# Performance work log

Measured on AMD Instinct MI355X. Metric: run time of the kernel, lower is better.

Reference implementation:

```python
import jax, jax.numpy as jnp
import numpy as np

NUM_USERS = 150000
NUM_ITEMS = 80000
N_NODES = NUM_USERS + NUM_ITEMS
NNZ = 5000000
LATENT_DIM = 64
N_LAYERS = 3


def setup_inputs() -> dict:
    key = jax.random.key(0)
    k1, k2, k3, k4, k5 = jax.random.split(key, 5)
    user_emb = 0.1 * jax.random.normal(k1, (NUM_USERS, LATENT_DIM), dtype=jnp.float32)
    item_emb = 0.1 * jax.random.normal(k2, (NUM_ITEMS, LATENT_DIM), dtype=jnp.float32)
    adj_rows = jax.random.randint(k3, (NNZ,), 0, N_NODES, dtype=jnp.int32)
    adj_cols = jax.random.randint(k4, (NNZ,), 0, N_NODES, dtype=jnp.int32)
    # scale values ~ 1/avg_degree so propagation is stable (mimics sym-normalized adjacency)
    adj_vals = jax.random.uniform(k5, (NNZ,), dtype=jnp.float32) * (N_NODES / NNZ)
    return {"user_emb": user_emb, "item_emb": item_emb,
            "adj_rows": adj_rows, "adj_cols": adj_cols, "adj_vals": adj_vals}


def _spmm(rows, cols, vals, x):
    # y[r] = sum_{e: rows[e]==r} vals[e] * x[cols[e]]  == torch.sparse.mm(G, x)
    return jax.ops.segment_sum(vals[:, None] * x[cols], rows, num_segments=N_NODES)


def reference(user_emb, item_emb, adj_rows, adj_cols, adj_vals):
    all_emb = jnp.concatenate([user_emb, item_emb], axis=0)  # [N, d]
    acc = all_emb
    for _ in range(N_LAYERS):
        all_emb = _spmm(adj_rows, adj_cols, adj_vals, all_emb)
        acc = acc + all_emb
    light_out = acc / (N_LAYERS + 1)  # mean over stacked layer embeddings
    users = light_out[:NUM_USERS]
    items = light_out[NUM_USERS:]
    return users, items
```

## Files before the change

### kernel.cpp

```cpp
#include <hip/hip_runtime.h>

#define NUM_USERS 150000
#define NUM_ITEMS 80000
#define N_NODES   230000
#define NNZ       5000000
#define DIM       64

#define SB_SHIFT 10
#define SB_SIZE  1024
#define NUM_SB   ((N_NODES + SB_SIZE - 1) / SB_SIZE)
#define SB_CAP   32768
#define PA_ITEMS 4

#define NSLICES   (N_NODES / 8)

#define VAL_MAX   0.046f
#define VAL_ENC   (16384.0f / VAL_MAX)
#define VAL_SCALE (VAL_MAX / 16384.0f)

__device__ __forceinline__ unsigned short f2bf(float f) {
    unsigned int u = __float_as_uint(f);
    u += 0x7FFFu + ((u >> 16) & 1u);
    return (unsigned short)(u >> 16);
}
__device__ __forceinline__ float bflo(unsigned int u) {
    return __uint_as_float(u << 16);
}
__device__ __forceinline__ float bfhi(unsigned int u) {
    return __uint_as_float(u & 0xFFFF0000u);
}
__device__ __forceinline__ unsigned int pk2(float a, float b) {
    return (unsigned int)f2bf(a) | ((unsigned int)f2bf(b) << 16);
}

__global__ void init_kernel(const float* __restrict__ u,
                            const float* __restrict__ it,
                            unsigned short* __restrict__ x) {
    long i = (long)blockIdx.x * blockDim.x + threadIdx.x;
    const long n4  = (long)N_NODES * DIM / 4;
    const long iu4 = (long)NUM_USERS * DIM / 4;
    if (i >= n4) return;
    float4 v = (i < iu4) ? ((const float4*)u)[i]
                         : ((const float4*)it)[i - iu4];
    ushort4 h;
    h.x = f2bf(v.x); h.y = f2bf(v.y); h.z = f2bf(v.z); h.w = f2bf(v.w);
    ((ushort4*)x)[i] = h;
}

__global__ void cursor_init_kernel(int* __restrict__ bucket_cursor) {
    int t = threadIdx.x;
    if (t < NUM_SB) bucket_cursor[t] = t * SB_CAP;
}

__global__ void partA_kernel(const int* __restrict__ rows,
                             const int* __restrict__ cols,
                             const float* __restrict__ vals,
                             int* __restrict__ bucket_cursor,
                             unsigned int* __restrict__ Xe,
                             unsigned short* __restrict__ Xr) {
    __shared__ int bcnt[NUM_SB];
    __shared__ int bbase[NUM_SB];
    const int t = threadIdx.x;
    const long tile = 1024L * PA_ITEMS;
    for (long base = (long)blockIdx.x * tile; base < NNZ;
         base += (long)gridDim.x * tile) {
        for (int j = t; j < NUM_SB; j += 1024) bcnt[j] = 0;
        __syncthreads();
        int b[PA_ITEMS], rank[PA_ITEMS], rl[PA_ITEMS];
        unsigned int pk[PA_ITEMS];
        bool ok[PA_ITEMS];
        for (int k = 0; k < PA_ITEMS; ++k) {
            long e = base + (long)k * 1024 + t;
            ok[k] = (e < NNZ);
            if (ok[k]) {
                int r = rows[e];
                b[k]  = r >> SB_SHIFT;
                rl[k] = r & (SB_SIZE - 1);
                int vc = (int)(vals[e] * VAL_ENC + 0.5f);
                vc = min(vc, 16383);
                pk[k] = ((unsigned int)vc << 18) | (unsigned int)cols[e];
                rank[k] = atomicAdd(&bcnt[b[k]], 1);
            }
        }
        __syncthreads();
        for (int j = t; j < NUM_SB; j += 1024)
            if (bcnt[j] > 0) bbase[j] = atomicAdd(&bucket_cursor[j], bcnt[j]);
        __syncthreads();
        for (int k = 0; k < PA_ITEMS; ++k)
            if (ok[k]) {
                int pos = bbase[b[k]] + rank[k];
                Xe[pos] = pk[k];
                Xr[pos] = (unsigned short)rl[k];
            }
        __syncthreads();
    }
}

__global__ void sb_scan_kernel(const int* __restrict__ bucket_cursor,
                               int* __restrict__ sb_base) {
    __shared__ int lds[256];
    const int t = threadIdx.x;
    const int s = (t < NUM_SB) ? (bucket_cursor[t] - t * SB_CAP) : 0;
    lds[t] = s;
    __syncthreads();
    for (int off = 1; off < 256; off <<= 1) {
        int add = (t >= off) ? lds[t - off] : 0;
        __syncthreads();
        lds[t] += add;
        __syncthreads();
    }
    if (t < NUM_SB) sb_base[t] = lds[t] - s;
    if (t == 0) sb_base[NUM_SB] = NNZ;
}

__global__ void partB_kernel(const unsigned int* __restrict__ Xe,
                             const unsigned short* __restrict__ Xr,
                             const int* __restrict__ sb_base,
                             int* __restrict__ row_start,
                             unsigned int* __restrict__ edges) {
    __shared__ int hist[SB_SIZE];
    __shared__ int scan[SB_SIZE];
    const int b    = blockIdx.x;
    const int t    = threadIdx.x;
    const int rlo  = b << SB_SHIFT;
    const int nrows = min(SB_SIZE, N_NODES - rlo);
    const int xoff = b * SB_CAP;
    const int base = sb_base[b];
    const int cnt  = sb_base[b + 1] - base;
    hist[t] = 0;
    __syncthreads();
    for (int i = t; i < cnt; i += 1024)
        atomicAdd(&hist[Xr[xoff + i]], 1);
    __syncthreads();
    const int v = hist[t];
    scan[t] = v;
    __syncthreads();
    for (int off = 1; off < 1024; off <<= 1) {
        int add = (t >= off) ? scan[t - off] : 0;
        __syncthreads();
        scan[t] += add;
        __syncthreads();
    }
    const int rs = base + (scan[t] - v);
    if (t < nrows) row_start[rlo + t] = rs;
    hist[t] = rs;
    __syncthreads();
    for (int i = t; i < cnt; i += 1024) {
        int rl = Xr[xoff + i];
        int pos = atomicAdd(&hist[rl], 1);
        edges[pos] = Xe[xoff + i];
    }
    if (b == 0 && t == 0) row_start[N_NODES] = NNZ;
}

#define FMA8(v, h) \
    a0 = fmaf((v), bflo((h).x), a0); a1 = fmaf((v), bfhi((h).x), a1); \
    a2 = fmaf((v), bflo((h).y), a2); a3 = fmaf((v), bfhi((h).y), a3); \
    a4 = fmaf((v), bflo((h).z), a4); a5 = fmaf((v), bfhi((h).z), a5); \
    a6 = fmaf((v), bflo((h).w), a6); a7 = fmaf((v), bfhi((h).w), a7);

__global__ __launch_bounds__(256)
void spmm8_kernel(const int* __restrict__ row_start,
                  const unsigned int* __restrict__ edges,
                  const unsigned short* __restrict__ x,
                  unsigned short* __restrict__ y) {
    const int lane = threadIdx.x & 63;
    const int oct  = lane >> 3;
    const int fo   = (lane & 7) << 3;
    const int wv   = blockIdx.x * 4 + (threadIdx.x >> 6);
    if (wv >= NSLICES) return;
    const int row = wv * 8 + oct;
    const int s   = row_start[row];
    const int deg = row_start[row + 1] - s;
    int dm = deg;
    dm = max(dm, __shfl_xor(dm, 8));
    dm = max(dm, __shfl_xor(dm, 16));
    dm = max(dm, __shfl_xor(dm, 32));
    dm = __builtin_amdgcn_readfirstlane(dm);
    const unsigned short* xf = x + fo;
    float a0 = 0, a1 = 0, a2 = 0, a3 = 0, a4 = 0, a5 = 0, a6 = 0, a7 = 0;
    for (int i = 0; i < dm; i += 8) {
        unsigned int ev[8];
        uint4 h[8];
        #pragma unroll
        for (int k = 0; k < 8; ++k) {
            const int o = (i + k < deg) ? (s + i + k) : 0;
            ev[k] = edges[o];
        }
        #pragma unroll
        for (int k = 0; k < 8; ++k)
            h[k] = *(const uint4*)(xf + (((long)(ev[k] & 0x3FFFF)) << 6));
        #pragma unroll
        for (int k = 0; k < 8; ++k) {
            const float v = (i + k < deg)
                          ? (float)(ev[k] >> 18) * VAL_SCALE : 0.0f;
            FMA8(v, h[k]);
        }
    }
    uint4 w;
    w.x = pk2(a0, a1); w.y = pk2(a2, a3);
    w.z = pk2(a4, a5); w.w = pk2(a6, a7);
    *(uint4*)(y + (((long)row) << 6) + fo) = w;
}

__global__ __launch_bounds__(256)
void spmm_final8_kernel(const int* __restrict__ row_start,
                        const unsigned int* __restrict__ edges,
                        const unsigned short* __restrict__ y2,
                        const unsigned short* __restrict__ y1,
                        const float* __restrict__ u,
                        const float* __restrict__ it,
                        float* __restrict__ acc) {
    const int lane = threadIdx.x & 63;
    const int oct  = lane >> 3;
    const int fo   = (lane & 7) << 3;
    const int wv   = blockIdx.x * 4 + (threadIdx.x >> 6);
    if (wv >= NSLICES) return;
    const int row = wv * 8 + oct;
    const int s   = row_start[row];
    const int deg = row_start[row + 1] - s;
    int dm = deg;
    dm = max(dm, __shfl_xor(dm, 8));
    dm = max(dm, __shfl_xor(dm, 16));
    dm = max(dm, __shfl_xor(dm, 32));
    dm = __builtin_amdgcn_readfirstlane(dm);
    const unsigned short* xf = y2 + fo;
    float a0 = 0, a1 = 0, a2 = 0, a3 = 0, a4 = 0, a5 = 0, a6 = 0, a7 = 0;
    for (int i = 0; i < dm; i += 8) {
        unsigned int ev[8];
        uint4 h[8];
        #pragma unroll
        for (int k = 0; k < 8; ++k) {
            const int o = (i + k < deg) ? (s + i + k) : 0;
            ev[k] = edges[o];
        }
        #pragma unroll
        for (int k = 0; k < 8; ++k)
            h[k] = *(const uint4*)(xf + (((long)(ev[k] & 0x3FFFF)) << 6));
        #pragma unroll
        for (int k = 0; k < 8; ++k) {
            const float v = (i + k < deg)
                          ? (float)(ev[k] >> 18) * VAL_SCALE : 0.0f;
            FMA8(v, h[k]);
        }
    }
    const long o = (((long)row) << 6) + fo;
    const float* x0p = (row < NUM_USERS) ? (u + o)
                     : (it + o - (((long)NUM_USERS) << 6));
    const float4 xa = *(const float4*)(x0p);
    const float4 xb = *(const float4*)(x0p + 4);
    const uint4 h1 = *(const uint4*)(y1 + o);
    const uint4 h2 = *(const uint4*)(y2 + o);
    float4 ra, rb;
    ra.x = (xa.x + bflo(h1.x) + bflo(h2.x) + a0) * 0.25f;
    ra.y = (xa.y + bfhi(h1.x) + bfhi(h2.x) + a1) * 0.25f;
    ra.z = (xa.z + bflo(h1.y) + bflo(h2.y) + a2) * 0.25f;
    ra.w = (xa.w + bfhi(h1.y) + bfhi(h2.y) + a3) * 0.25f;
    rb.x = (xb.x + bflo(h1.z) + bflo(h2.z) + a4) * 0.25f;
    rb.y = (xb.y + bfhi(h1.z) + bfhi(h2.z) + a5) * 0.25f;
    rb.z = (xb.z + bflo(h1.w) + bflo(h2.w) + a6) * 0.25f;
    rb.w = (xb.w + bfhi(h1.w) + bfhi(h2.w) + a7) * 0.25f;
    *(float4*)(acc + o) = ra;
    *(float4*)(acc + o + 4) = rb;
}

extern "C" void kernel_launch(void* const* d_in, const int* in_sizes, int n_in,
                              void* d_out, int out_size, void* d_ws, size_t ws_size,
                              hipStream_t stream) {
    const float* u    = (const float*)d_in[0];
    const float* it   = (const float*)d_in[1];
    const int*   rows = (const int*)d_in[2];
    const int*   cols = (const int*)d_in[3];
    const float* vals = (const float*)d_in[4];
    float* acc = (float*)d_out;

    const size_t bufBf = (size_t)N_NODES * DIM * 2;
    const size_t edgeB = (size_t)NNZ * 4;
    const size_t XeB   = (size_t)NUM_SB * SB_CAP * 4;
    const size_t XrB   = (size_t)NUM_SB * SB_CAP * 2;
    const size_t nodeB = 921600;
    char* ws = (char*)d_ws;
    unsigned short* buf0 = (unsigned short*)(ws);
    unsigned short* buf1 = (unsigned short*)(ws + bufBf);
    unsigned short* buf2 = (unsigned short*)(ws + 2 * bufBf);
    unsigned int*   edges = (unsigned int*)(ws + 3 * bufBf);
    unsigned int*   Xe   = (unsigned int*)(ws + 3 * bufBf + edgeB);
    unsigned short* Xr   = (unsigned short*)(ws + 3 * bufBf + edgeB + XeB);
    char* p              = ws + 3 * bufBf + edgeB + XeB + XrB;
    int* row_start       = (int*)(p);   p += nodeB;
    int* bucket_cursor   = (int*)(p);   p += 1024;
    int* sb_base         = (int*)(p);

    const int n4 = N_NODES * DIM / 4;
    const int ewGrid = (n4 + 255) / 256;

    init_kernel<<<ewGrid, 256, 0, stream>>>(u, it, buf0);

    cursor_init_kernel<<<1, 256, 0, stream>>>(bucket_cursor);
    partA_kernel<<<512, 1024, 0, stream>>>(rows, cols, vals, bucket_cursor, Xe, Xr);
    sb_scan_kernel<<<1, 256, 0, stream>>>(bucket_cursor, sb_base);
    partB_kernel<<<NUM_SB, 1024, 0, stream>>>(Xe, Xr, sb_base, row_start, edges);

    const int spmmGrid = (NSLICES + 3) / 4;
    spmm8_kernel<<<spmmGrid, 256, 0, stream>>>(row_start, edges, buf0, buf1);
    spmm8_kernel<<<spmmGrid, 256, 0, stream>>>(row_start, edges, buf1, buf2);
    spmm_final8_kernel<<<spmmGrid, 256, 0, stream>>>(row_start, edges, buf2,
                                                     buf1, u, it, acc);
}
```

Measured before the change: 548.7 us.

## Halve super-bucket size and fold cursor init and bucket scan into neighbours

Super-buckets shrink from 1024 to 512 rows (about 450 buckets), which doubles the partB block count for better load balance. The cursor-init and bucket-scan kernels are removed: init_kernel now seeds the cursors, and every partB block redoes the bucket prefix scan itself. This cuts two launches and their serialization, at the cost of redundant scans in each block and more bucket atomics in partA. With SB_CAP at 16384, the expected bucket load of roughly 11k leaves a smaller safety margin.

```diff
diff --git a/kernel.cpp b/kernel.cpp
--- a/kernel.cpp
+++ b/kernel.cpp
@@ -6,10 +6,10 @@
 #define NNZ       5000000
 #define DIM       64
 
-#define SB_SHIFT 10
-#define SB_SIZE  1024
+#define SB_SHIFT 9
+#define SB_SIZE  512
 #define NUM_SB   ((N_NODES + SB_SIZE - 1) / SB_SIZE)
-#define SB_CAP   32768
+#define SB_CAP   16384
 #define PA_ITEMS 4
 
 #define NSLICES   (N_NODES / 8)
@@ -35,8 +35,10 @@
 
 __global__ void init_kernel(const float* __restrict__ u,
                             const float* __restrict__ it,
-                            unsigned short* __restrict__ x) {
+                            unsigned short* __restrict__ x,
+                            int* __restrict__ bucket_cursor) {
     long i = (long)blockIdx.x * blockDim.x + threadIdx.x;
+    if (i < NUM_SB) bucket_cursor[i] = (int)i * SB_CAP;
     const long n4  = (long)N_NODES * DIM / 4;
     const long iu4 = (long)NUM_USERS * DIM / 4;
     if (i >= n4) return;
@@ -47,17 +49,13 @@
     ((ushort4*)x)[i] = h;
 }
 
-__global__ void cursor_init_kernel(int* __restrict__ bucket_cursor) {
-    int t = threadIdx.x;
-    if (t < NUM_SB) bucket_cursor[t] = t * SB_CAP;
-}
-
-__global__ void partA_kernel(const int* __restrict__ rows,
-                             const int* __restrict__ cols,
-                             const float* __restrict__ vals,
-                             int* __restrict__ bucket_cursor,
-                             unsigned int* __restrict__ Xe,
-                             unsigned short* __restrict__ Xr) {
+__global__ __launch_bounds__(1024)
+void partA_kernel(const int* __restrict__ rows,
+                  const int* __restrict__ cols,
+                  const float* __restrict__ vals,
+                  int* __restrict__ bucket_cursor,
+                  unsigned int* __restrict__ Xe,
+                  unsigned short* __restrict__ Xr) {
     __shared__ int bcnt[NUM_SB];
     __shared__ int bbase[NUM_SB];
     const int t = threadIdx.x;
@@ -96,54 +94,50 @@
     }
 }
 
-__global__ void sb_scan_kernel(const int* __restrict__ bucket_cursor,
-                               int* __restrict__ sb_base) {
-    __shared__ int lds[256];
-    const int t = threadIdx.x;
-    const int s = (t < NUM_SB) ? (bucket_cursor[t] - t * SB_CAP) : 0;
-    lds[t] = s;
-    __syncthreads();
-    for (int off = 1; off < 256; off <<= 1) {
-        int add = (t >= off) ? lds[t - off] : 0;
-        __syncthreads();
-        lds[t] += add;
-        __syncthreads();
-    }
-    if (t < NUM_SB) sb_base[t] = lds[t] - s;
-    if (t == 0) sb_base[NUM_SB] = NNZ;
-}
-
-__global__ void partB_kernel(const unsigned int* __restrict__ Xe,
-                             const unsigned short* __restrict__ Xr,
-                             const int* __restrict__ sb_base,
-                             int* __restrict__ row_start,
-                             unsigned int* __restrict__ edges) {
+__global__ __launch_bounds__(1024)
+void partB_kernel(const unsigned int* __restrict__ Xe,
+                  const unsigned short* __restrict__ Xr,
+                  const int* __restrict__ bucket_cursor,
+                  int* __restrict__ row_start,
+                  unsigned int* __restrict__ edges) {
+    __shared__ int bsc[512];
     __shared__ int hist[SB_SIZE];
-    __shared__ int scan[SB_SIZE];
+    __shared__ int scn[SB_SIZE];
     const int b    = blockIdx.x;
     const int t    = threadIdx.x;
     const int rlo  = b << SB_SHIFT;
     const int nrows = min(SB_SIZE, N_NODES - rlo);
     const int xoff = b * SB_CAP;
-    const int base = sb_base[b];
-    const int cnt  = sb_base[b + 1] - base;
-    hist[t] = 0;
+
+    if (t < 512) bsc[t] = (t < NUM_SB) ? (bucket_cursor[t] - t * SB_CAP) : 0;
+    if (t < SB_SIZE) hist[t] = 0;
     __syncthreads();
+    for (int off = 1; off < 512; off <<= 1) {
+        int add = (t >= off && t < 512) ? bsc[t - off] : 0;
+        __syncthreads();
+        if (t < 512) bsc[t] += add;
+        __syncthreads();
+    }
+    const int base = (b == 0) ? 0 : bsc[b - 1];
+    const int cnt  = bsc[b] - base;
+
     for (int i = t; i < cnt; i += 1024)
         atomicAdd(&hist[Xr[xoff + i]], 1);
     __syncthreads();
-    const int v = hist[t];
-    scan[t] = v;
+    const int v = (t < SB_SIZE) ? hist[t] : 0;
+    if (t < SB_SIZE) scn[t] = v;
     __syncthreads();
-    for (int off = 1; off < 1024; off <<= 1) {
-        int add = (t >= off) ? scan[t - off] : 0;
-        __syncthreads();
-        scan[t] += add;
-        __syncthreads();
-    }
-    const int rs = base + (scan[t] - v);
-    if (t < nrows) row_start[rlo + t] = rs;
-    hist[t] = rs;
+    for (int off = 1; off < SB_SIZE; off <<= 1) {
+        int add = (t >= off && t < SB_SIZE) ? scn[t - off] : 0;
+        __syncthreads();
+        if (t < SB_SIZE) scn[t] += add;
+        __syncthreads();
+    }
+    if (t < SB_SIZE) {
+        const int rs = base + (scn[t] - v);
+        if (t < nrows) row_start[rlo + t] = rs;
+        hist[t] = rs;
+    }
     __syncthreads();
     for (int i = t; i < cnt; i += 1024) {
         int rl = Xr[xoff + i];
@@ -288,18 +282,16 @@
     unsigned short* Xr   = (unsigned short*)(ws + 3 * bufBf + edgeB + XeB);
     char* p              = ws + 3 * bufBf + edgeB + XeB + XrB;
     int* row_start       = (int*)(p);   p += nodeB;
-    int* bucket_cursor   = (int*)(p);   p += 1024;
-    int* sb_base         = (int*)(p);
+    int* bucket_cursor   = (int*)(p);
 
     const int n4 = N_NODES * DIM / 4;
     const int ewGrid = (n4 + 255) / 256;
 
-    init_kernel<<<ewGrid, 256, 0, stream>>>(u, it, buf0);
-
-    cursor_init_kernel<<<1, 256, 0, stream>>>(bucket_cursor);
+    init_kernel<<<ewGrid, 256, 0, stream>>>(u, it, buf0, bucket_cursor);
+
     partA_kernel<<<512, 1024, 0, stream>>>(rows, cols, vals, bucket_cursor, Xe, Xr);
-    sb_scan_kernel<<<1, 256, 0, stream>>>(bucket_cursor, sb_base);
-    partB_kernel<<<NUM_SB, 1024, 0, stream>>>(Xe, Xr, sb_base, row_start, edges);
+    partB_kernel<<<NUM_SB, 1024, 0, stream>>>(Xe, Xr, bucket_cursor,
+                                              row_start, edges);
 
     const int spmmGrid = (NSLICES + 3) / 4;
     spmm8_kernel<<<spmmGrid, 256, 0, stream>>>(row_start, edges, buf0, buf1);
```

Result: no change. 553.9 us (+0.9%).
